# Kernel optimization log

Measured on AMD Instinct MI355X. Metric: run time of the kernel, lower is better.

The kernel has to match this reference:

```python
import jax, jax.numpy as jnp
from jax import lax
import numpy as np

L, B, D_IN, D_OUT, D_MLP = 64, 32, 512, 512, 128
WINDOWS = [1, 3]
FEATS = [256, 128]
C = sum(FEATS)  # 384
EPS = 1e-5


def _leaky(x):
    return jnp.where(x >= 0, x, 0.1 * x)


def setup_inputs() -> dict:
    key = jax.random.key(0)
    ks = jax.random.split(key, 16)
    s = lambda k, shp: (jax.random.normal(k, shp, jnp.float32) * 0.02)
    inp = {}
    inp["x"] = jax.random.normal(ks[0], (L, B, D_IN), jnp.float32)
    inp["xs_mask"] = jnp.ones((L, B), jnp.float32)
    # conv + batchnorm params per window
    inp["conv_w0"] = s(ks[1], (FEATS[0], 1, D_IN * WINDOWS[0]))
    inp["conv_b0"] = jnp.zeros((FEATS[0],), jnp.float32)
    inp["gamma0"] = jnp.ones((FEATS[0],), jnp.float32)
    inp["beta0"] = jnp.zeros((FEATS[0],), jnp.float32)
    inp["conv_w1"] = s(ks[2], (FEATS[1], 1, D_IN * WINDOWS[1]))
    inp["conv_b1"] = jnp.zeros((FEATS[1],), jnp.float32)
    inp["gamma1"] = jnp.ones((FEATS[1],), jnp.float32)
    inp["beta1"] = jnp.zeros((FEATS[1],), jnp.float32)
    inp["w0"] = s(ks[3], (2 * C, D_MLP)); inp["b0"] = jnp.zeros((D_MLP,), jnp.float32)
    inp["w1"] = s(ks[4], (D_MLP, D_MLP)); inp["b1"] = jnp.zeros((D_MLP,), jnp.float32)
    inp["w2"] = s(ks[5], (D_MLP, D_MLP)); inp["b2"] = jnp.zeros((D_MLP,), jnp.float32)
    inp["w3"] = s(ks[6], (D_MLP, D_MLP)); inp["b3"] = jnp.zeros((D_MLP,), jnp.float32)
    # output MLP: Linear(d_mlp->d_mlp), Linear(d_mlp->d_out)
    inp["w4"] = s(ks[7], (D_MLP, D_MLP)); inp["b4"] = jnp.zeros((D_MLP,), jnp.float32)
    inp["w5"] = s(ks[8], (D_MLP, D_OUT)); inp["b5"] = jnp.zeros((D_OUT,), jnp.float32)
    return inp


def reference(x, xs_mask, conv_w0, conv_b0, gamma0, beta0, conv_w1, conv_b1,
              gamma1, beta1, w0, b0, w1, b1, w2, b2, w3, b3, w4, b4, w5, b5):
    # x: (L, B, E)
    x = x * xs_mask[:, :, None]
    xf = jnp.transpose(x, (1, 0, 2)).reshape(B, 1, L * D_IN)  # (B, 1, L*E)

    # CNN front-end: Conv1d(stride=d_in) + BatchNorm1d (batch stats) + LeakyReLU
    feats = []
    for win, cw, cb, g, bt in [(WINDOWS[0], conv_w0, conv_b0, gamma0, beta0),
                               (WINDOWS[1], conv_w1, conv_b1, gamma1, beta1)]:
        pad = (win - 1) // 2 * D_IN
        y = lax.conv_general_dilated(xf, cw, window_strides=(D_IN,),
                                     padding=[(pad, pad)],
                                     dimension_numbers=("NCH", "OIH", "NCH"))
        y = y + cb[None, :, None]  # (B, C_k, L)
        m = y.mean(axis=(0, 2))
        v = y.var(axis=(0, 2))  # biased var, as torch BN training mode
        y = (y - m[None, :, None]) / jnp.sqrt(v[None, :, None] + EPS)
        y = y * g[None, :, None] + bt[None, :, None]
        feats.append(_leaky(y))
    h = jnp.concatenate(feats, axis=1)          # (B, C, L)
    h = jnp.transpose(h, (2, 0, 1))             # (L, B, C)
    h = h * xs_mask[:, :, None]

    # Graph propagation: pairwise concat + first linear, split over concat halves
    # cat([h_i, h_j]) @ w0 == h_i @ w0[:C] + h_j @ w0[C:]  (avoids (L,L,B,2C) tensor)
    a = jnp.einsum("lbc,cd->lbd", h, w0[:C])    # (L, B, d_mlp)
    bb = jnp.einsum("lbc,cd->lbd", h, w0[C:])   # (L, B, d_mlp)
    p = _leaky(a[:, None, :, :] + bb[None, :, :, :] + b0)  # (L, L, B, d_mlp)
    p = _leaky(p @ w1 + b1)
    p = _leaky(p @ w2 + b2)
    p = _leaky(p @ w3 + b3)
    p = p * xs_mask[:, None, :, None]
    p = p.mean(axis=1)                          # (L, B, d_mlp)

    out = _leaky(p @ w4 + b4)
    out = _leaky(out @ w5 + b5)                 # (L, B, d_out)
    return out * xs_mask[:, :, None]
```

## Files before the change

kernel.cpp:

```cpp
#include <hip/hip_runtime.h>


#define BB 32
#define CCH 384

__device__ __forceinline__ float leaky(float x) { return fmaxf(x, 0.1f * x); }

typedef _Float16 f16x8 __attribute__((ext_vector_type(8)));
typedef float f32x4 __attribute__((ext_vector_type(4)));

union F8u { uint32_t u[4]; uint4 q; f16x8 h; };

__device__ __forceinline__ uint32_t pack2(float x) {
  _Float16 hi = (_Float16)x;
  _Float16 lo = (_Float16)((x - (float)hi) * 2048.0f);
  union { _Float16 f[2]; uint32_t u; } p;
  p.f[0] = hi; p.f[1] = lo;
  return p.u;
}

#define SEL_LO 0x05040100u
#define SEL_HI 0x07060302u

__global__ __launch_bounds__(256) void conv_kernel(
    const float* __restrict__ x, const float* __restrict__ mask,
    const float* __restrict__ cw0, const float* __restrict__ cw1,
    float* __restrict__ yG)
{
  __shared__ float As[32 * 36];
  __shared__ float Ws[32 * 132];
  int bx = blockIdx.x;
  int rt = bx & 63;
  int ct = bx >> 6;
  int row0 = rt * 32;
  int tid = threadIdx.x;

  const float* wbase; int wstride;
  if (ct < 2) { wbase = cw0 + ct * 128 * 512; wstride = 512; }
  else        { wbase = cw1 + (ct - 2) * 512; wstride = 1536; }

  int sr  = tid >> 3;
  int sk4 = (tid & 7) * 4;
  const float* xrow = x + (row0 + sr) * 512;
  float mval = mask[row0 + sr];

  int r4 = (tid >> 5) * 4;
  int c4 = (tid & 31) * 4;

  float acc[4][4] = {{0.f,0.f,0.f,0.f},{0.f,0.f,0.f,0.f},
                     {0.f,0.f,0.f,0.f},{0.f,0.f,0.f,0.f}};
#pragma unroll 1
  for (int k0 = 0; k0 < 512; k0 += 32) {
    float4 xv = *(const float4*)(xrow + k0 + sk4);
    float4 wv[4];
#pragma unroll
    for (int rep = 0; rep < 4; ++rep) {
      int slot = rep * 256 + tid;
      int c = slot >> 3;
      int kq4 = (slot & 7) * 4;
      wv[rep] = *(const float4*)(wbase + c * wstride + k0 + kq4);
    }
    __syncthreads();
    As[(sk4 + 0) * 36 + sr] = xv.x * mval;
    As[(sk4 + 1) * 36 + sr] = xv.y * mval;
    As[(sk4 + 2) * 36 + sr] = xv.z * mval;
    As[(sk4 + 3) * 36 + sr] = xv.w * mval;
#pragma unroll
    for (int rep = 0; rep < 4; ++rep) {
      int slot = rep * 256 + tid;
      int c = slot >> 3;
      int kq4 = (slot & 7) * 4;
      Ws[(kq4 + 0) * 132 + c] = wv[rep].x;
      Ws[(kq4 + 1) * 132 + c] = wv[rep].y;
      Ws[(kq4 + 2) * 132 + c] = wv[rep].z;
      Ws[(kq4 + 3) * 132 + c] = wv[rep].w;
    }
    __syncthreads();
#pragma unroll
    for (int kk = 0; kk < 32; ++kk) {
      float4 a = *(const float4*)&As[kk * 36 + r4];
      float4 w = *(const float4*)&Ws[kk * 132 + c4];
      float av[4] = {a.x, a.y, a.z, a.w};
      float wv2[4] = {w.x, w.y, w.z, w.w};
#pragma unroll
      for (int ri = 0; ri < 4; ++ri)
#pragma unroll
        for (int ci = 0; ci < 4; ++ci)
          acc[ri][ci] = fmaf(av[ri], wv2[ci], acc[ri][ci]);
    }
  }
#pragma unroll
  for (int ci = 0; ci < 4; ++ci)
    *(float4*)&yG[(ct * 128 + c4 + ci) * 2048 + row0 + r4] =
        make_float4(acc[0][ci], acc[1][ci], acc[2][ci], acc[3][ci]);
}

__global__ __launch_bounds__(256) void stats_kernel(
    const float* __restrict__ yG,
    const float* __restrict__ g0, const float* __restrict__ be0,
    const float* __restrict__ g1, const float* __restrict__ be1,
    float* __restrict__ scale, float* __restrict__ shift)
{
  int c = blockIdx.x;
  int tid = threadIdx.x;
  float s = 0.f, s2 = 0.f;
  if (c < 256) {
    const float* src = yG + c * 2048 + tid * 8;
    float4 v0 = *(const float4*)(src);
    float4 v1 = *(const float4*)(src + 4);
    s  = v0.x + v0.y + v0.z + v0.w + v1.x + v1.y + v1.z + v1.w;
    s2 = v0.x*v0.x + v0.y*v0.y + v0.z*v0.z + v0.w*v0.w
       + v1.x*v1.x + v1.y*v1.y + v1.z*v1.z + v1.w*v1.w;
  } else {
    int cc = c - 256;
    const float* p0 = yG + (256 + cc) * 2048;
    const float* p1 = yG + (384 + cc) * 2048;
    const float* p2 = yG + (512 + cc) * 2048;
#pragma unroll
    for (int j = 0; j < 8; ++j) {
      int e = tid * 8 + j;
      float v = p1[e];
      if (e >= 32)   v += p0[e - 32];
      if (e < 2016)  v += p2[e + 32];
      s += v; s2 += v * v;
    }
  }
#pragma unroll
  for (int off = 32; off > 0; off >>= 1) {
    s  += __shfl_down(s, off);
    s2 += __shfl_down(s2, off);
  }
  __shared__ float rs[4], rs2[4];
  int wid = tid >> 6;
  if ((tid & 63) == 0) { rs[wid] = s; rs2[wid] = s2; }
  __syncthreads();
  if (tid == 0) {
    float S  = rs[0] + rs[1] + rs[2] + rs[3];
    float S2 = rs2[0] + rs2[1] + rs2[2] + rs2[3];
    float mean = S * (1.f / 2048.f);
    float var  = S2 * (1.f / 2048.f) - mean * mean;
    float g  = (c < 256) ? g0[c] : g1[c - 256];
    float be = (c < 256) ? be0[c] : be1[c - 256];
    float sc = g / sqrtf(var + 1e-5f);
    scale[c] = sc;
    shift[c] = be - mean * sc;
  }
}

__global__ __launch_bounds__(256) void ab_kernel(
    const float* __restrict__ yG, const float* __restrict__ scale,
    const float* __restrict__ shift, const float* __restrict__ mask,
    const float* __restrict__ w0,
    float* __restrict__ a_arr, float* __restrict__ bb_arr)
{
  __shared__ float As[32 * 36];
  __shared__ float Ws[32 * 68];
  int bx = blockIdx.x;
  int rt = bx & 63, ct = bx >> 6;
  int row0 = rt * 32, n0 = ct * 64;
  int tid = threadIdx.x;
  int r4 = (tid >> 5) * 4;
  int n2 = (tid & 31) * 2;
  int scc = tid >> 3, srr4 = (tid & 7) * 4;
  int wnn8 = (tid & 7) * 8;
  const float* wbase = (n0 < 128) ? (w0 + n0) : (w0 + CCH * 128 + (n0 - 128));
  float4 mv = *(const float4*)(mask + row0 + srr4);

  float acc[4][2] = {{0.f, 0.f}};
#pragma unroll 1
  for (int c0 = 0; c0 < 384; c0 += 32) {
    int c = c0 + scc;
    float4 yv;
    if (c < 256) {
      yv = *(const float4*)(yG + c * 2048 + row0 + srr4);
    } else {
      int cc = c - 256;
      yv = *(const float4*)(yG + (384 + cc) * 2048 + row0 + srr4);
      if (rt > 0) {
        float4 u = *(const float4*)(yG + (256 + cc) * 2048 + row0 + srr4 - 32);
        yv.x += u.x; yv.y += u.y; yv.z += u.z; yv.w += u.w;
      }
      if (rt < 63) {
        float4 u = *(const float4*)(yG + (512 + cc) * 2048 + row0 + srr4 + 32);
        yv.x += u.x; yv.y += u.y; yv.z += u.z; yv.w += u.w;
      }
    }
    float sc = scale[c], sh = shift[c];
    float4 wv0 = *(const float4*)(wbase + c * 128 + wnn8);
    float4 wv1 = *(const float4*)(wbase + c * 128 + wnn8 + 4);
    __syncthreads();
    float4 hv;
    hv.x = leaky(fmaf(yv.x, sc, sh)) * mv.x;
    hv.y = leaky(fmaf(yv.y, sc, sh)) * mv.y;
    hv.z = leaky(fmaf(yv.z, sc, sh)) * mv.z;
    hv.w = leaky(fmaf(yv.w, sc, sh)) * mv.w;
    *(float4*)&As[scc * 36 + srr4] = hv;
    *(float4*)&Ws[scc * 68 + wnn8] = wv0;
    *(float4*)&Ws[scc * 68 + wnn8 + 4] = wv1;
    __syncthreads();
#pragma unroll
    for (int cc = 0; cc < 32; ++cc) {
      float4 a = *(const float4*)&As[cc * 36 + r4];
      float2 w = *(const float2*)&Ws[cc * 68 + n2];
      acc[0][0] = fmaf(a.x, w.x, acc[0][0]); acc[0][1] = fmaf(a.x, w.y, acc[0][1]);
      acc[1][0] = fmaf(a.y, w.x, acc[1][0]); acc[1][1] = fmaf(a.y, w.y, acc[1][1]);
      acc[2][0] = fmaf(a.z, w.x, acc[2][0]); acc[2][1] = fmaf(a.z, w.y, acc[2][1]);
      acc[3][0] = fmaf(a.w, w.x, acc[3][0]); acc[3][1] = fmaf(a.w, w.y, acc[3][1]);
    }
  }
  float* dst; int nd;
  if (n0 < 128) { dst = a_arr; nd = n0; } else { dst = bb_arr; nd = n0 - 128; }
#pragma unroll
  for (int ri = 0; ri < 4; ++ri)
    *(float2*)&dst[(row0 + r4 + ri) * 128 + nd + n2] = make_float2(acc[ri][0], acc[ri][1]);
}

__global__ __launch_bounds__(256) void wsplit_kernel(
    const float* __restrict__ w1, const float* __restrict__ w2,
    const float* __restrict__ w3, uint32_t* __restrict__ wpk)
{
  int e = blockIdx.x * 256 + threadIdx.x;
  int L = e >> 14;
  int r = e & 16383;
  int k = r >> 7, n = r & 127;
  const float* w = (L == 0) ? w1 : (L == 1) ? w2 : w3;
  wpk[L * 16384 + n * 128 + k] = pack2(w[k * 128 + n]);
}

__global__ __launch_bounds__(256) void pair_kernel(
    const float* __restrict__ a_arr, const float* __restrict__ bb_arr,
    const float* __restrict__ b0, const uint32_t* __restrict__ wpk,
    const float* __restrict__ b1, const float* __restrict__ b2,
    const float* __restrict__ b3,
    const float* __restrict__ mask, float* __restrict__ pmean)
{
  __shared__ uint32_t Apk[128 * 132];
  int i = blockIdx.x, bp = blockIdx.y;
  int tid = threadIdx.x;

#pragma unroll 1
  for (int it = 0; it < 16; ++it) {
    int idx = it * 256 + tid;
    int r   = idx >> 5;
    int k4  = (idx & 31) * 4;
    int db  = r >> 6, j = r & 63;
    int bq  = bp * 2 + db;
    float4 av = *(const float4*)(a_arr + (i * BB + bq) * 128 + k4);
    float4 bv = *(const float4*)(bb_arr + (j * BB + bq) * 128 + k4);
    float4 zv = *(const float4*)(b0 + k4);
    uint4 w;
    w.x = pack2(leaky(av.x + bv.x + zv.x));
    w.y = pack2(leaky(av.y + bv.y + zv.y));
    w.z = pack2(leaky(av.z + bv.z + zv.z));
    w.w = pack2(leaky(av.w + bv.w + zv.w));
    *(uint4*)&Apk[r * 132 + k4] = w;
  }
  __syncthreads();

  int wid = __builtin_amdgcn_readfirstlane(tid >> 6);
  int wm = wid & 1, wn = wid >> 1;
  int lane = tid & 63;
  int m16 = lane & 15, q = lane >> 4;

  f32x4 hi[4][4], cr[4][4];

#pragma unroll 1
  for (int L = 0; L < 3; ++L) {
    const uint32_t* Wg = wpk + L * 16384;
    const float* Bv = (L == 0) ? b1 : (L == 1) ? b2 : b3;
#pragma unroll
    for (int mt = 0; mt < 4; ++mt)
#pragma unroll
      for (int nt = 0; nt < 4; ++nt) {
        hi[mt][nt] = (f32x4){0.f, 0.f, 0.f, 0.f};
        cr[mt][nt] = (f32x4){0.f, 0.f, 0.f, 0.f};
      }

#pragma unroll 1
    for (int ks = 0; ks < 4; ++ks) {
      int koff = ks * 32 + q * 8;
      F8u Wh[4], Wl[4];
#pragma unroll
      for (int nt = 0; nt < 4; ++nt) {
        const uint32_t* p = Wg + (wn * 64 + nt * 16 + m16) * 128 + koff;
        uint4 ra = *(const uint4*)p;
        uint4 rb = *(const uint4*)(p + 4);
        Wh[nt].u[0] = __builtin_amdgcn_perm(ra.y, ra.x, SEL_LO);
        Wh[nt].u[1] = __builtin_amdgcn_perm(ra.w, ra.z, SEL_LO);
        Wh[nt].u[2] = __builtin_amdgcn_perm(rb.y, rb.x, SEL_LO);
        Wh[nt].u[3] = __builtin_amdgcn_perm(rb.w, rb.z, SEL_LO);
        Wl[nt].u[0] = __builtin_amdgcn_perm(ra.y, ra.x, SEL_HI);
        Wl[nt].u[1] = __builtin_amdgcn_perm(ra.w, ra.z, SEL_HI);
        Wl[nt].u[2] = __builtin_amdgcn_perm(rb.y, rb.x, SEL_HI);
        Wl[nt].u[3] = __builtin_amdgcn_perm(rb.w, rb.z, SEL_HI);
      }
#pragma unroll
      for (int mt = 0; mt < 4; ++mt) {
        const uint32_t* ap = &Apk[(wm * 64 + mt * 16 + m16) * 132 + koff];
        uint4 ra = *(const uint4*)ap;
        uint4 rb = *(const uint4*)(ap + 4);
        F8u Ah, Al;
        Ah.u[0] = __builtin_amdgcn_perm(ra.y, ra.x, SEL_LO);
        Ah.u[1] = __builtin_amdgcn_perm(ra.w, ra.z, SEL_LO);
        Ah.u[2] = __builtin_amdgcn_perm(rb.y, rb.x, SEL_LO);
        Ah.u[3] = __builtin_amdgcn_perm(rb.w, rb.z, SEL_LO);
        Al.u[0] = __builtin_amdgcn_perm(ra.y, ra.x, SEL_HI);
        Al.u[1] = __builtin_amdgcn_perm(ra.w, ra.z, SEL_HI);
        Al.u[2] = __builtin_amdgcn_perm(rb.y, rb.x, SEL_HI);
        Al.u[3] = __builtin_amdgcn_perm(rb.w, rb.z, SEL_HI);
#pragma unroll
        for (int nt = 0; nt < 4; ++nt) {
          hi[mt][nt] = __builtin_amdgcn_mfma_f32_16x16x32_f16(
              Ah.h, Wh[nt].h, hi[mt][nt], 0, 0, 0);
          cr[mt][nt] = __builtin_amdgcn_mfma_f32_16x16x32_f16(
              Ah.h, Wl[nt].h, cr[mt][nt], 0, 0, 0);
          cr[mt][nt] = __builtin_amdgcn_mfma_f32_16x16x32_f16(
              Al.h, Wh[nt].h, cr[mt][nt], 0, 0, 0);
        }
      }
    }

    float bias[4];
#pragma unroll
    for (int nt = 0; nt < 4; ++nt) bias[nt] = Bv[wn * 64 + nt * 16 + m16];

    if (L < 2) {
      __syncthreads();
#pragma unroll
      for (int mt = 0; mt < 4; ++mt)
#pragma unroll
        for (int nt = 0; nt < 4; ++nt)
#pragma unroll
          for (int rg = 0; rg < 4; ++rg) {
            float d = leaky(hi[mt][nt][rg] + cr[mt][nt][rg] * (1.0f / 2048.0f)
                            + bias[nt]);
            int row = wm * 64 + mt * 16 + q * 4 + rg;
            Apk[row * 132 + wn * 64 + nt * 16 + m16] = pack2(d);
          }
      __syncthreads();
    } else {
      float s[4] = {0.f, 0.f, 0.f, 0.f};
#pragma unroll
      for (int nt = 0; nt < 4; ++nt)
#pragma unroll
        for (int mt = 0; mt < 4; ++mt)
#pragma unroll
          for (int rg = 0; rg < 4; ++rg)
            s[nt] += leaky(hi[mt][nt][rg] + cr[mt][nt][rg] * (1.0f / 2048.0f)
                           + bias[nt]);
      int brow = i * BB + bp * 2 + wm;
      float mfac = (1.0f / 64.0f) * mask[brow];
#pragma unroll
      for (int nt = 0; nt < 4; ++nt) {
        s[nt] += __shfl_xor(s[nt], 16, 64);
        s[nt] += __shfl_xor(s[nt], 32, 64);
      }
      if (lane < 16) {
#pragma unroll
        for (int nt = 0; nt < 4; ++nt)
          pmean[brow * 128 + wn * 64 + nt * 16 + m16] = s[nt] * mfac;
      }
    }
  }
}

__global__ __launch_bounds__(256) void out_kernel(
    const float* __restrict__ pmean, const float* __restrict__ w4,
    const float* __restrict__ b4, const float* __restrict__ w5,
    const float* __restrict__ b5, const float* __restrict__ mask,
    float* __restrict__ out)
{
  __shared__ float Pm[16 * 132];
  __shared__ float T4[16 * 132];
  int bx = blockIdx.x;
  int col0 = (bx & 1) * 256;
  int row0 = (bx >> 1) * 16;
  int tid = threadIdx.x;
  int tr = tid >> 4, m = tid & 15;

  {
    const float* src = pmean + (row0 + tr) * 128 + 8 * m;
    *(float4*)&Pm[tr * 132 + 8 * m]     = *(const float4*)(src);
    *(float4*)&Pm[tr * 132 + 8 * m + 4] = *(const float4*)(src + 4);
  }
  __syncthreads();
  {
    int k8 = m * 8;
    float4 bv0 = *(const float4*)(b4 + k8);
    float4 bv1 = *(const float4*)(b4 + k8 + 4);
    float t[8] = {bv0.x, bv0.y, bv0.z, bv0.w, bv1.x, bv1.y, bv1.z, bv1.w};
#pragma unroll 4
    for (int cc = 0; cc < 128; ++cc) {
      float a = Pm[tr * 132 + cc];
      float4 w0v = *(const float4*)(w4 + cc * 128 + k8);
      float4 w1v = *(const float4*)(w4 + cc * 128 + k8 + 4);
      t[0] = fmaf(a, w0v.x, t[0]); t[1] = fmaf(a, w0v.y, t[1]);
      t[2] = fmaf(a, w0v.z, t[2]); t[3] = fmaf(a, w0v.w, t[3]);
      t[4] = fmaf(a, w1v.x, t[4]); t[5] = fmaf(a, w1v.y, t[5]);
      t[6] = fmaf(a, w1v.z, t[6]); t[7] = fmaf(a, w1v.w, t[7]);
    }
    *(float4*)&T4[tr * 132 + k8]     = make_float4(leaky(t[0]), leaky(t[1]), leaky(t[2]), leaky(t[3]));
    *(float4*)&T4[tr * 132 + k8 + 4] = make_float4(leaky(t[4]), leaky(t[5]), leaky(t[6]), leaky(t[7]));
  }
  __syncthreads();
  {
    int c16 = m * 16;
    const float* bsrc = b5 + col0 + c16;
    float o[16];
#pragma unroll
    for (int qq = 0; qq < 4; ++qq) {
      float4 bv = *(const float4*)(bsrc + 4 * qq);
      o[4*qq+0] = bv.x; o[4*qq+1] = bv.y; o[4*qq+2] = bv.z; o[4*qq+3] = bv.w;
    }
#pragma unroll 2
    for (int cc = 0; cc < 128; ++cc) {
      float a = T4[tr * 132 + cc];
      const float* wr = w5 + cc * 512 + col0 + c16;
#pragma unroll
      for (int qq = 0; qq < 4; ++qq) {
        float4 wv = *(const float4*)(wr + 4 * qq);
        o[4*qq+0] = fmaf(a, wv.x, o[4*qq+0]);
        o[4*qq+1] = fmaf(a, wv.y, o[4*qq+1]);
        o[4*qq+2] = fmaf(a, wv.z, o[4*qq+2]);
        o[4*qq+3] = fmaf(a, wv.w, o[4*qq+3]);
      }
    }
    float mv = mask[row0 + tr];
    float* dst = out + (row0 + tr) * 512 + col0 + c16;
#pragma unroll
    for (int qq = 0; qq < 4; ++qq)
      *(float4*)(dst + 4 * qq) = make_float4(leaky(o[4*qq+0]) * mv, leaky(o[4*qq+1]) * mv,
                                             leaky(o[4*qq+2]) * mv, leaky(o[4*qq+3]) * mv);
  }
}

extern "C" void kernel_launch(void* const* d_in, const int* in_sizes, int n_in,
                              void* d_out, int out_size, void* d_ws, size_t ws_size,
                              hipStream_t stream) {
  const float* x    = (const float*)d_in[0];
  const float* mask = (const float*)d_in[1];
  const float* cw0  = (const float*)d_in[2];
  const float* g0   = (const float*)d_in[4];
  const float* be0  = (const float*)d_in[5];
  const float* cw1  = (const float*)d_in[6];
  const float* g1   = (const float*)d_in[8];
  const float* be1  = (const float*)d_in[9];
  const float* w0   = (const float*)d_in[10];
  const float* b0   = (const float*)d_in[11];
  const float* w1   = (const float*)d_in[12];
  const float* b1   = (const float*)d_in[13];
  const float* w2   = (const float*)d_in[14];
  const float* b2   = (const float*)d_in[15];
  const float* w3   = (const float*)d_in[16];
  const float* b3   = (const float*)d_in[17];
  const float* w4   = (const float*)d_in[18];
  const float* b4   = (const float*)d_in[19];
  const float* w5   = (const float*)d_in[20];
  const float* b5   = (const float*)d_in[21];

  float* ws     = (float*)d_ws;
  float* yG     = ws;
  float* pmean  = ws;
  uint32_t* wpk = (uint32_t*)(ws + 262144);
  float* scale  = ws + 1310720;
  float* shift  = ws + 1311104;
  float* a_arr  = ws + 1311488;
  float* bb_arr = ws + 1573632;
  float* outp   = (float*)d_out;

  conv_kernel<<<320, 256, 0, stream>>>(x, mask, cw0, cw1, yG);
  stats_kernel<<<384, 256, 0, stream>>>(yG, g0, be0, g1, be1, scale, shift);
  ab_kernel<<<256, 256, 0, stream>>>(yG, scale, shift, mask, w0, a_arr, bb_arr);
  wsplit_kernel<<<192, 256, 0, stream>>>(w1, w2, w3, wpk);
  dim3 g5(64, 16);
  pair_kernel<<<g5, 256, 0, stream>>>(a_arr, bb_arr, b0, wpk, b1, b2, b3,
                                      mask, pmean);
  out_kernel<<<256, 256, 0, stream>>>(pmean, w4, b4, w5, b5, mask, outp);
}
```

Measured before the change: 295.6 us.

## Store fp16 hi/lo split planes separately and use 8 waves in pair kernel

The packed hi/lo fp16 interleaved layout is replaced by separate hi and lo planes, for both the LDS activation tile and the pre-split weights. MFMA operands now load directly as uint4 without the byte-permute unpacking. The pair kernel moves to 512 threads, so each wave covers half as many output columns, and the next k-slice of weights is prefetched into registers. The epilogue pairs lanes with a shuffle so each lane writes one packed half2 word, which costs extra shuffle and select work in exchange for fewer ALU ops and lower register pressure per wave.

Result: faster. 285.7 us (-3.3%).

```diff
diff --git a/kernel.cpp b/kernel.cpp
--- a/kernel.cpp
+++ b/kernel.cpp
@@ -9,18 +9,17 @@
 typedef _Float16 f16x8 __attribute__((ext_vector_type(8)));
 typedef float f32x4 __attribute__((ext_vector_type(4)));
 
-union F8u { uint32_t u[4]; uint4 q; f16x8 h; };
-
-__device__ __forceinline__ uint32_t pack2(float x) {
-  _Float16 hi = (_Float16)x;
-  _Float16 lo = (_Float16)((x - (float)hi) * 2048.0f);
-  union { _Float16 f[2]; uint32_t u; } p;
-  p.f[0] = hi; p.f[1] = lo;
-  return p.u;
-}
-
-#define SEL_LO 0x05040100u
-#define SEL_HI 0x07060302u
+union F8 { uint4 q; f16x8 h; };
+union H2 { _Float16 f[2]; uint32_t u; };
+
+__device__ __forceinline__ void split2(float d0, float d1,
+                                       uint32_t& hw, uint32_t& lw) {
+  H2 h, l;
+  h.f[0] = (_Float16)d0; h.f[1] = (_Float16)d1;
+  l.f[0] = (_Float16)((d0 - (float)h.f[0]) * 2048.0f);
+  l.f[1] = (_Float16)((d1 - (float)h.f[1]) * 2048.0f);
+  hw = h.u; lw = l.u;
+}
 
 __global__ __launch_bounds__(256) void conv_kernel(
     const float* __restrict__ x, const float* __restrict__ mask,
@@ -220,40 +219,57 @@
     const float* __restrict__ w3, uint32_t* __restrict__ wpk)
 {
   int e = blockIdx.x * 256 + threadIdx.x;
-  int L = e >> 14;
-  int r = e & 16383;
-  int k = r >> 7, n = r & 127;
+  int L = e >> 13;
+  int r = e & 8191;
+  int k2 = r >> 7, n = r & 127;
+  int k = k2 * 2;
   const float* w = (L == 0) ? w1 : (L == 1) ? w2 : w3;
-  wpk[L * 16384 + n * 128 + k] = pack2(w[k * 128 + n]);
-}
-
-__global__ __launch_bounds__(256) void pair_kernel(
+  uint32_t hw, lw;
+  split2(w[k * 128 + n], w[(k + 1) * 128 + n], hw, lw);
+  wpk[L * 8192 + n * 64 + k2] = hw;
+  wpk[24576 + L * 8192 + n * 64 + k2] = lw;
+}
+
+__global__ __launch_bounds__(512) void pair_kernel(
     const float* __restrict__ a_arr, const float* __restrict__ bb_arr,
     const float* __restrict__ b0, const uint32_t* __restrict__ wpk,
     const float* __restrict__ b1, const float* __restrict__ b2,
     const float* __restrict__ b3,
     const float* __restrict__ mask, float* __restrict__ pmean)
 {
-  __shared__ uint32_t Apk[128 * 132];
+  __shared__ uint32_t Ahs[128 * 68];
+  __shared__ uint32_t Als[128 * 68];
   int i = blockIdx.x, bp = blockIdx.y;
   int tid = threadIdx.x;
 
 #pragma unroll 1
-  for (int it = 0; it < 16; ++it) {
-    int idx = it * 256 + tid;
-    int r   = idx >> 5;
-    int k4  = (idx & 31) * 4;
+  for (int it = 0; it < 4; ++it) {
+    int idx = it * 512 + tid;
+    int r   = idx >> 4;
+    int k8  = (idx & 15) * 8;
     int db  = r >> 6, j = r & 63;
     int bq  = bp * 2 + db;
-    float4 av = *(const float4*)(a_arr + (i * BB + bq) * 128 + k4);
-    float4 bv = *(const float4*)(bb_arr + (j * BB + bq) * 128 + k4);
-    float4 zv = *(const float4*)(b0 + k4);
-    uint4 w;
-    w.x = pack2(leaky(av.x + bv.x + zv.x));
-    w.y = pack2(leaky(av.y + bv.y + zv.y));
-    w.z = pack2(leaky(av.z + bv.z + zv.z));
-    w.w = pack2(leaky(av.w + bv.w + zv.w));
-    *(uint4*)&Apk[r * 132 + k4] = w;
+    const float* ap = a_arr + (i * BB + bq) * 128 + k8;
+    const float* bbp = bb_arr + (j * BB + bq) * 128 + k8;
+    const float* zp = b0 + k8;
+    float d[8];
+#pragma unroll
+    for (int t = 0; t < 8; t += 4) {
+      float4 av = *(const float4*)(ap + t);
+      float4 bv = *(const float4*)(bbp + t);
+      float4 zv = *(const float4*)(zp + t);
+      d[t+0] = leaky(av.x + bv.x + zv.x);
+      d[t+1] = leaky(av.y + bv.y + zv.y);
+      d[t+2] = leaky(av.z + bv.z + zv.z);
+      d[t+3] = leaky(av.w + bv.w + zv.w);
+    }
+    uint4 hq, lq;
+    split2(d[0], d[1], hq.x, lq.x);
+    split2(d[2], d[3], hq.y, lq.y);
+    split2(d[4], d[5], hq.z, lq.z);
+    split2(d[6], d[7], hq.w, lq.w);
+    *(uint4*)&Ahs[r * 68 + k8 / 2] = hq;
+    *(uint4*)&Als[r * 68 + k8 / 2] = lq;
   }
   __syncthreads();
 
@@ -262,54 +278,48 @@
   int lane = tid & 63;
   int m16 = lane & 15, q = lane >> 4;
 
-  f32x4 hi[4][4], cr[4][4];
+  f32x4 hi[4][2], cr[4][2];
 
 #pragma unroll 1
   for (int L = 0; L < 3; ++L) {
-    const uint32_t* Wg = wpk + L * 16384;
+    const uint32_t* WhL = wpk + L * 8192;
+    const uint32_t* WlL = wpk + 24576 + L * 8192;
     const float* Bv = (L == 0) ? b1 : (L == 1) ? b2 : b3;
 #pragma unroll
     for (int mt = 0; mt < 4; ++mt)
 #pragma unroll
-      for (int nt = 0; nt < 4; ++nt) {
+      for (int nt = 0; nt < 2; ++nt) {
         hi[mt][nt] = (f32x4){0.f, 0.f, 0.f, 0.f};
         cr[mt][nt] = (f32x4){0.f, 0.f, 0.f, 0.f};
       }
 
+    F8 Wh[2], Wl[2], Whn[2], Wln[2];
+#pragma unroll
+    for (int nt = 0; nt < 2; ++nt) {
+      int wrow = wn * 32 + nt * 16 + m16;
+      Wh[nt].q = *(const uint4*)(WhL + wrow * 64 + q * 4);
+      Wl[nt].q = *(const uint4*)(WlL + wrow * 64 + q * 4);
+    }
+
 #pragma unroll 1
     for (int ks = 0; ks < 4; ++ks) {
-      int koff = ks * 32 + q * 8;
-      F8u Wh[4], Wl[4];
-#pragma unroll
-      for (int nt = 0; nt < 4; ++nt) {
-        const uint32_t* p = Wg + (wn * 64 + nt * 16 + m16) * 128 + koff;
-        uint4 ra = *(const uint4*)p;
-        uint4 rb = *(const uint4*)(p + 4);
-        Wh[nt].u[0] = __builtin_amdgcn_perm(ra.y, ra.x, SEL_LO);
-        Wh[nt].u[1] = __builtin_amdgcn_perm(ra.w, ra.z, SEL_LO);
-        Wh[nt].u[2] = __builtin_amdgcn_perm(rb.y, rb.x, SEL_LO);
-        Wh[nt].u[3] = __builtin_amdgcn_perm(rb.w, rb.z, SEL_LO);
-        Wl[nt].u[0] = __builtin_amdgcn_perm(ra.y, ra.x, SEL_HI);
-        Wl[nt].u[1] = __builtin_amdgcn_perm(ra.w, ra.z, SEL_HI);
-        Wl[nt].u[2] = __builtin_amdgcn_perm(rb.y, rb.x, SEL_HI);
-        Wl[nt].u[3] = __builtin_amdgcn_perm(rb.w, rb.z, SEL_HI);
+      int koff2 = ks * 16 + q * 4;
+      if (ks < 3) {
+#pragma unroll
+        for (int nt = 0; nt < 2; ++nt) {
+          int wrow = wn * 32 + nt * 16 + m16;
+          Whn[nt].q = *(const uint4*)(WhL + wrow * 64 + koff2 + 16);
+          Wln[nt].q = *(const uint4*)(WlL + wrow * 64 + koff2 + 16);
+        }
       }
 #pragma unroll
       for (int mt = 0; mt < 4; ++mt) {
-        const uint32_t* ap = &Apk[(wm * 64 + mt * 16 + m16) * 132 + koff];
-        uint4 ra = *(const uint4*)ap;
-        uint4 rb = *(const uint4*)(ap + 4);
-        F8u Ah, Al;
-        Ah.u[0] = __builtin_amdgcn_perm(ra.y, ra.x, SEL_LO);
-        Ah.u[1] = __builtin_amdgcn_perm(ra.w, ra.z, SEL_LO);
-        Ah.u[2] = __builtin_amdgcn_perm(rb.y, rb.x, SEL_LO);
-        Ah.u[3] = __builtin_amdgcn_perm(rb.w, rb.z, SEL_LO);
-        Al.u[0] = __builtin_amdgcn_perm(ra.y, ra.x, SEL_HI);
-        Al.u[1] = __builtin_amdgcn_perm(ra.w, ra.z, SEL_HI);
-        Al.u[2] = __builtin_amdgcn_perm(rb.y, rb.x, SEL_HI);
-        Al.u[3] = __builtin_amdgcn_perm(rb.w, rb.z, SEL_HI);
-#pragma unroll
-        for (int nt = 0; nt < 4; ++nt) {
+        int arow = wm * 64 + mt * 16 + m16;
+        F8 Ah, Al;
+        Ah.q = *(const uint4*)&Ahs[arow * 68 + koff2];
+        Al.q = *(const uint4*)&Als[arow * 68 + koff2];
+#pragma unroll
+        for (int nt = 0; nt < 2; ++nt) {
           hi[mt][nt] = __builtin_amdgcn_mfma_f32_16x16x32_f16(
               Ah.h, Wh[nt].h, hi[mt][nt], 0, 0, 0);
           cr[mt][nt] = __builtin_amdgcn_mfma_f32_16x16x32_f16(
@@ -318,30 +328,41 @@
               Al.h, Wh[nt].h, cr[mt][nt], 0, 0, 0);
         }
       }
-    }
-
-    float bias[4];
-#pragma unroll
-    for (int nt = 0; nt < 4; ++nt) bias[nt] = Bv[wn * 64 + nt * 16 + m16];
+#pragma unroll
+      for (int nt = 0; nt < 2; ++nt) { Wh[nt] = Whn[nt]; Wl[nt] = Wln[nt]; }
+    }
+
+    float bias[2];
+#pragma unroll
+    for (int nt = 0; nt < 2; ++nt) bias[nt] = Bv[wn * 32 + nt * 16 + m16];
 
     if (L < 2) {
       __syncthreads();
+      int par = lane & 1;
 #pragma unroll
       for (int mt = 0; mt < 4; ++mt)
 #pragma unroll
-        for (int nt = 0; nt < 4; ++nt)
+        for (int nt = 0; nt < 2; ++nt) {
+          int colw = (wn * 32 + nt * 16 + (m16 & ~1)) >> 1;
 #pragma unroll
           for (int rg = 0; rg < 4; ++rg) {
             float d = leaky(hi[mt][nt][rg] + cr[mt][nt][rg] * (1.0f / 2048.0f)
                             + bias[nt]);
+            float dn = __shfl_xor(d, 1, 64);
+            float de = par ? dn : d;
+            float do_ = par ? d : dn;
+            uint32_t hw, lw;
+            split2(de, do_, hw, lw);
             int row = wm * 64 + mt * 16 + q * 4 + rg;
-            Apk[row * 132 + wn * 64 + nt * 16 + m16] = pack2(d);
+            if (par) Als[row * 68 + colw] = lw;
+            else     Ahs[row * 68 + colw] = hw;
           }
+        }
       __syncthreads();
     } else {
-      float s[4] = {0.f, 0.f, 0.f, 0.f};
-#pragma unroll
-      for (int nt = 0; nt < 4; ++nt)
+      float s[2] = {0.f, 0.f};
+#pragma unroll
+      for (int nt = 0; nt < 2; ++nt)
 #pragma unroll
         for (int mt = 0; mt < 4; ++mt)
 #pragma unroll
@@ -351,14 +372,14 @@
       int brow = i * BB + bp * 2 + wm;
       float mfac = (1.0f / 64.0f) * mask[brow];
 #pragma unroll
-      for (int nt = 0; nt < 4; ++nt) {
+      for (int nt = 0; nt < 2; ++nt) {
         s[nt] += __shfl_xor(s[nt], 16, 64);
         s[nt] += __shfl_xor(s[nt], 32, 64);
       }
       if (lane < 16) {
 #pragma unroll
-        for (int nt = 0; nt < 4; ++nt)
-          pmean[brow * 128 + wn * 64 + nt * 16 + m16] = s[nt] * mfac;
+        for (int nt = 0; nt < 2; ++nt)
+          pmean[brow * 128 + wn * 32 + nt * 16 + m16] = s[nt] * mfac;
       }
     }
   }
@@ -471,9 +492,9 @@
   conv_kernel<<<320, 256, 0, stream>>>(x, mask, cw0, cw1, yG);
   stats_kernel<<<384, 256, 0, stream>>>(yG, g0, be0, g1, be1, scale, shift);
   ab_kernel<<<256, 256, 0, stream>>>(yG, scale, shift, mask, w0, a_arr, bb_arr);
-  wsplit_kernel<<<192, 256, 0, stream>>>(w1, w2, w3, wpk);
+  wsplit_kernel<<<96, 256, 0, stream>>>(w1, w2, w3, wpk);
   dim3 g5(64, 16);
-  pair_kernel<<<g5, 256, 0, stream>>>(a_arr, bb_arr, b0, wpk, b1, b2, b3,
+  pair_kernel<<<g5, 512, 0, stream>>>(a_arr, bb_arr, b0, wpk, b1, b2, b3,
                                       mask, pmean);
   out_kernel<<<256, 256, 0, stream>>>(pmean, w4, b4, w5, b5, mask, outp);
 }
```
